# Kernel tuning notes

Hardware: AMD Instinct MI355X
Metric: run time of the kernel (lower is better)

The kernel has to match this reference:

```python
import jax, jax.numpy as jnp
import numpy as np

# Regular batched tree: BS roots, arity A, depth D (root=level 0, leaves=level D)
BS, A, D = 32, 4, 6
V, E, H = 50000, 256, 256
LEVEL_SIZES = [BS * A ** d for d in range(D + 1)]
OFFSETS = np.concatenate([[0], np.cumsum(LEVEL_SIZES)]).astype(np.int64)
TOTAL = int(OFFSETS[-1])  # 174752


def gru_cell(x, h, w_ih, w_hh, b_ih, b_hh):
    # torch nn.GRU single step, gate order (r, z, n)
    gi = x @ w_ih.T + b_ih
    gh = h @ w_hh.T + b_hh
    ir, iz, inn = jnp.split(gi, 3, axis=-1)
    hr, hz, hn = jnp.split(gh, 3, axis=-1)
    r = jax.nn.sigmoid(ir + hr)
    z = jax.nn.sigmoid(iz + hz)
    n = jnp.tanh(inn + r * hn)
    return (1.0 - z) * n + z * h


def child_attention(h_last, sent_weight, sent_bias, context_weight):
    # Reproduces hidden_per_child stacking: ch[g,c,i,:] = h_last[g,c] if c==i else 0.
    G, S, _ = h_last.shape
    eye = jnp.eye(S, dtype=h_last.dtype)
    ch = h_last[:, :, None, :] * eye[None, :, :, None]          # [G,S(c),S(i),H]
    t1 = jnp.tanh(jnp.einsum('gcih,hk->gcik', ch, sent_weight) + sent_bias[0])
    u = jnp.tanh(jnp.einsum('gcik,ko->gci', t1, context_weight))  # [G,S,S]
    w = jax.nn.softmax(u, axis=1)                                # softmax over c (the P axis)
    return jnp.einsum('gci,gcih->gih', w, ch)                    # [G,S,H]


def setup_inputs() -> dict:
    key = jax.random.key(0)
    ks = jax.random.split(key, 9)
    s = 1.0 / np.sqrt(H)
    return {
        'tokens': jax.random.randint(ks[0], (TOTAL,), 0, V, dtype=jnp.int32),
        'embedding': jax.random.normal(ks[1], (V, E), jnp.float32) * 0.1,
        'w_ih': jax.random.uniform(ks[2], (3 * H, E), jnp.float32, -s, s),
        'w_hh': jax.random.uniform(ks[3], (3 * H, H), jnp.float32, -s, s),
        'b_ih': jax.random.uniform(ks[4], (3 * H,), jnp.float32, -s, s),
        'b_hh': jax.random.uniform(ks[5], (3 * H,), jnp.float32, -s, s),
        'sent_weight': jax.random.normal(ks[6], (H, H), jnp.float32) * 0.05,
        'sent_bias': jax.random.normal(ks[7], (1, H), jnp.float32) * 0.05,
        'context_weight': jax.random.normal(ks[8], (H, 1), jnp.float32) * 0.05,
    }


def reference(tokens, embedding, w_ih, w_hh, b_ih, b_hh, sent_weight, sent_bias, context_weight):
    def tok(d):
        return tokens[int(OFFSETS[d]):int(OFFSETS[d + 1])]

    gru = lambda x, h: gru_cell(x, h, w_ih, w_hh, b_ih, b_hh)

    # leaves: no children -> zero initial hidden
    h_levels = {D: gru(embedding[tok(D)], jnp.zeros((LEVEL_SIZES[D], H), jnp.float32))}

    for d in range(D - 1, -1, -1):
        h_child = h_levels[d + 1].reshape(-1, A, H)   # [N_d, A, H]
        # duplicate index_copy in torch: only last child's hidden survives per parent
        h_last = h_child[:, A - 1, :]                 # [N_d, H]
        S = BS if d == 0 else A                       # call size: bs at root, A siblings otherwise
        groups = h_last.reshape(-1, S, H)
        chs = child_attention(groups, sent_weight, sent_bias, context_weight).reshape(-1, H)
        h_levels[d] = gru(embedding[tok(d)], chs)

    # final max over node_list: root entry has all bs rows; every other call's entry has
    # only row b = hn of the LAST sibling (duplicate valid_indices), zeros elsewhere.
    out = jnp.maximum(jnp.zeros((BS, H), jnp.float32), h_levels[0])
    for d in range(1, D + 1):
        last_sib = h_levels[d].reshape(BS, -1, A, H)[:, :, A - 1, :].max(axis=1)
        out = jnp.maximum(out, last_sib)
    return out
```

## Files before the change

kernel.cpp:

```cpp
#include <hip/hip_runtime.h>
#include <hip/hip_bf16.h>
#include <math.h>


typedef unsigned short u16;
typedef unsigned int u32;
typedef __attribute__((ext_vector_type(8))) short s8;
typedef __attribute__((ext_vector_type(4))) float f4;
#define MFMA16(a, b, c) __builtin_amdgcn_mfma_f32_16x16x32_bf16(a, b, c, 0, 0, 0)

__device__ __forceinline__ u16 f2bf(float f) {
  u32 x = __float_as_uint(f);
  return (u16)((x + 0x7fffu + ((x >> 16) & 1u)) >> 16);
}
__device__ __forceinline__ float bf2f(u16 u) { return __uint_as_float(((u32)u) << 16); }
__device__ __forceinline__ float sigmoidf_(float x) {
  return __builtin_amdgcn_rcpf(1.f + __builtin_amdgcn_exp2f(-1.4426950408889634f * x));
}
__device__ __forceinline__ float tanhf_(float x) {
  x = fminf(fmaxf(x, -15.f), 15.f);
  float t = __builtin_amdgcn_exp2f(-2.8853900817779268f * x);
  return 1.f - 2.f * t * __builtin_amdgcn_rcpf(1.f + t);
}
__device__ __forceinline__ void gload_lds16(const void* g, void* l) {
  typedef const __attribute__((address_space(1))) unsigned int* gp_t;
  typedef __attribute__((address_space(3))) unsigned int* lp_t;
  __builtin_amdgcn_global_load_lds((gp_t)g, (lp_t)l, 16, 0, 0);
}
__device__ __forceinline__ void stage_row(const float* __restrict__ emb, int tok,
                                          u16* aX, int r, int lane) {
  float4 v = ((const float4*)(emb + (size_t)tok * 256))[lane];
  uint2 val = {(u32)f2bf(v.x) | ((u32)f2bf(v.y) << 16),
               (u32)f2bf(v.z) | ((u32)f2bf(v.w) << 16)};
  *(uint2*)&aX[r * 256 + ((((lane >> 1)) ^ (r & 7)) << 3) + (lane & 1) * 4] = val;
}

__global__ void prep_pack(const float* __restrict__ wih, const float* __restrict__ whh,
                          const float* __restrict__ sw, const float* __restrict__ sb,
                          const float* __restrict__ cw,
                          u16* __restrict__ wihP, u16* __restrict__ whhPh,
                          u16* __restrict__ whhPl, u16* __restrict__ swPh,
                          float* __restrict__ u0p, int* __restrict__ outI) {
  int b = blockIdx.x, t = threadIdx.x;
  if (b == 320) {
    #pragma unroll
    for (int k = 0; k < 32; ++k) outI[k * 256 + t] = 0;
    if (t < 64) {
      float s = 0.f;
      #pragma unroll
      for (int q = 0; q < 4; ++q) { int k = t + 64 * q; s += tanhf(sb[k]) * cw[k]; }
      #pragma unroll
      for (int off = 32; off >= 1; off >>= 1) s += __shfl_xor(s, off);
      if (t == 0) u0p[0] = tanhf(s);
    }
    return;
  }
  int g = b * 256 + t;
  const float* src;
  u16* dst;
  int idx, NF, lomode, trans;
  if (g < 24576)      { idx = g;         src = wih; dst = wihP;  NF = 48; lomode = 0; trans = 1; }
  else if (g < 49152) { idx = g - 24576; src = whh; dst = whhPh; NF = 48; lomode = 0; trans = 1; }
  else if (g < 73728) { idx = g - 49152; src = whh; dst = whhPl; NF = 48; lomode = 1; trans = 1; }
  else                { idx = g - 73728; src = sw;  dst = swPh;  NF = 16; lomode = 0; trans = 0; }
  int lane = idx & 63;
  int t2 = idx >> 6;
  int nf = t2 % NF, kb = t2 / NF;
  int n = nf * 16 + (lane & 15);
  int k0 = kb * 32 + (lane >> 4) * 8;
  float v[8];
  if (trans) {
    const float4* p = (const float4*)(src + (size_t)n * 256 + k0);
    float4 a = p[0], b2 = p[1];
    v[0] = a.x; v[1] = a.y; v[2] = a.z; v[3] = a.w;
    v[4] = b2.x; v[5] = b2.y; v[6] = b2.z; v[7] = b2.w;
  } else {
    #pragma unroll
    for (int j = 0; j < 8; ++j) v[j] = src[(size_t)(k0 + j) * 256 + n];
  }
  u16 o[8];
  #pragma unroll
  for (int j = 0; j < 8; ++j) {
    u16 hi = f2bf(v[j]);
    o[j] = lomode ? f2bf(v[j] - bf2f(hi)) : hi;
  }
  u32* d = (u32*)(dst + (size_t)idx * 8);
  #pragma unroll
  for (int j = 0; j < 4; ++j) d[j] = (u32)o[2 * j] | ((u32)o[2 * j + 1] << 16);
}

__global__ __launch_bounds__(512, 2)
void levelAB_kernel(const int* __restrict__ t6, const int* __restrict__ t5,
                    const float* __restrict__ emb,
                    const u16* __restrict__ wihP, const u16* __restrict__ whhPh,
                    const u16* __restrict__ whhPl, const u16* __restrict__ swPh,
                    const float* __restrict__ bih, const float* __restrict__ bhh,
                    const float* __restrict__ sb, const float* __restrict__ cw,
                    const float* __restrict__ u0p,
                    u16* __restrict__ Hs5Hi, u16* __restrict__ Hs5Lo,
                    int* __restrict__ outI) {
  __shared__ u16 aX6[32768];
  __shared__ u16 aX5[8192];
  __shared__ u16 aH[2][8192];
  __shared__ float pm[8][32];
  __shared__ float scl[32];

  const int t = threadIdx.x;
  const int rb = blockIdx.x;
  const int lane = t & 63, w = t >> 6;
  const int asub = lane >> 4, l15 = lane & 15;
  const float LN3 = 1.0986122886681098f;
  const int batch = rb >> 3;

  {
    #pragma unroll
    for (int rr = 0; rr < 16; ++rr) {
      int r = 16 * w + rr;
      stage_row(emb, t6[4 * (128 * rb + r) + 3], aX6, r, lane);
    }
    #pragma unroll
    for (int rr = 0; rr < 4; ++rr) {
      int r = 4 * w + rr;
      stage_row(emb, t5[4 * (32 * rb + r) + 3], aX5, r, lane);
    }
  }
  __syncthreads();

  #pragma unroll 1
  for (int pass = 0; pass < 4; ++pass) {
    const int sp = pass >> 1, jc = pass & 1;
    const int cfx = 2 * w + jc;
    f4 gi[3][4];
    #pragma unroll
    for (int g = 0; g < 3; ++g)
      #pragma unroll
      for (int mf = 0; mf < 4; ++mf) gi[g][mf] = (f4){0.f, 0.f, 0.f, 0.f};
    s8 bw[2][3];
    auto LB = [&](int kb, int pb) {
      #pragma unroll
      for (int g = 0; g < 3; ++g)
        bw[pb][g] = *(const s8*)&wihP[((size_t)(kb * 48 + 16 * g + cfx) * 64 + lane) * 8];
    };
    LB(0, 0);
    #pragma unroll
    for (int kb = 0; kb < 8; ++kb) {
      const int pb = kb & 1;
      if (kb < 7) LB(kb + 1, pb ^ 1);
      s8 axh[4];
      #pragma unroll
      for (int mf = 0; mf < 4; ++mf) {
        int ab = (64 * sp + 16 * mf + l15) * 256 + (((kb * 4 + asub) ^ (l15 & 7)) << 3);
        axh[mf] = *(const s8*)&aX6[ab];
      }
      #pragma unroll
      for (int g = 0; g < 3; ++g)
        #pragma unroll
        for (int mf = 0; mf < 4; ++mf)
          gi[g][mf] = MFMA16(axh[mf], bw[pb][g], gi[g][mf]);
    }
    const int col = 16 * cfx + l15;
    const float bi0 = bih[col], bi1 = bih[256 + col], bi2 = bih[512 + col];
    const float bh0 = bhh[col], bh1 = bhh[256 + col], bh2 = bhh[512 + col];
    float cm = -1e30f;
    #pragma unroll
    for (int mf = 0; mf < 4; ++mf) {
      #pragma unroll
      for (int j = 0; j < 4; ++j) {
        float r = sigmoidf_(gi[0][mf][j] + bi0 + bh0);
        float z = sigmoidf_(gi[1][mf][j] + bi1 + bh1);
        float n = tanhf_(gi[2][mf][j] + bi2 + r * bh2);
        float h = (1.f - z) * n;
        if (j == 3) {
          int ci = 16 * sp + 4 * mf + asub;
          u16 hi = f2bf(h);
          u16 lo = f2bf(h - bf2f(hi));
          int hidx = ((col >> 3) * 32 + ci) * 8 + (col & 7);
          aH[0][hidx] = hi;
          aH[1][hidx] = lo;
        }
        cm = fmaxf(cm, h);
      }
    }
    cm = fmaxf(cm, __shfl_xor(cm, 16));
    cm = fmaxf(cm, __shfl_xor(cm, 32));
    if (asub == 0)
      atomicMax(outI + (size_t)batch * 256 + col, __float_as_int(cm));
  }
  __syncthreads();

  f4 sa[2][2];
  #pragma unroll
  for (int jc = 0; jc < 2; ++jc)
    #pragma unroll
    for (int mf = 0; mf < 2; ++mf) sa[jc][mf] = (f4){0.f, 0.f, 0.f, 0.f};
  {
    s8 bsw[2][2];
    auto LSW = [&](int kb, int pb) {
      #pragma unroll
      for (int jc = 0; jc < 2; ++jc)
        bsw[pb][jc] = *(const s8*)&swPh[((size_t)(kb * 16 + 2 * w + jc) * 64 + lane) * 8];
    };
    LSW(0, 0);
    #pragma unroll
    for (int kb = 0; kb < 8; ++kb) {
      const int pb = kb & 1;
      if (kb < 7) LSW(kb + 1, pb ^ 1);
      s8 ahh[2], ahl[2];
      #pragma unroll
      for (int mf = 0; mf < 2; ++mf) {
        int ab = ((kb * 4 + asub) * 32 + 16 * mf + l15) * 8;
        ahh[mf] = *(const s8*)&aH[0][ab];
        ahl[mf] = *(const s8*)&aH[1][ab];
      }
      #pragma unroll
      for (int jc = 0; jc < 2; ++jc) {
        sa[jc][0] = MFMA16(ahh[0], bsw[pb][jc], sa[jc][0]);
        sa[jc][1] = MFMA16(ahh[1], bsw[pb][jc], sa[jc][1]);
        sa[jc][0] = MFMA16(ahl[0], bsw[pb][jc], sa[jc][0]);
        sa[jc][1] = MFMA16(ahl[1], bsw[pb][jc], sa[jc][1]);
      }
    }
  }
  {
    float part[2][4] = {{0.f, 0.f, 0.f, 0.f}, {0.f, 0.f, 0.f, 0.f}};
    #pragma unroll
    for (int jc = 0; jc < 2; ++jc) {
      int k = 16 * (2 * w + jc) + l15;
      float sbk = sb[k], cwk = cw[k];
      #pragma unroll
      for (int mf = 0; mf < 2; ++mf)
        #pragma unroll
        for (int j = 0; j < 4; ++j) part[mf][j] += tanhf_(sa[jc][mf][j] + sbk) * cwk;
    }
    #pragma unroll
    for (int mf = 0; mf < 2; ++mf)
      #pragma unroll
      for (int j = 0; j < 4; ++j) {
        part[mf][j] += __shfl_xor(part[mf][j], 1);
        part[mf][j] += __shfl_xor(part[mf][j], 2);
        part[mf][j] += __shfl_xor(part[mf][j], 4);
        part[mf][j] += __shfl_xor(part[mf][j], 8);
      }
    if (l15 == 0) {
      #pragma unroll
      for (int mf = 0; mf < 2; ++mf)
        #pragma unroll
        for (int j = 0; j < 4; ++j) pm[w][16 * mf + 4 * asub + j] = part[mf][j];
    }
    __syncthreads();
    if (t < 32) {
      float v = 0.f;
      #pragma unroll
      for (int q = 0; q < 8; ++q) v += pm[q][t];
      scl[t] = sigmoidf_(tanhf_(v) - u0p[0] - LN3);
    }
    __syncthreads();
  }
  #pragma unroll 1
  for (int pass = 0; pass < 4; ++pass) {
    const int p = pass >> 1, mf = pass & 1;
    const int cf = w + 8 * p;
    f4 gi5[3], gh5[3];
    #pragma unroll
    for (int g = 0; g < 3; ++g) {
      gi5[g] = (f4){0.f, 0.f, 0.f, 0.f};
      gh5[g] = (f4){0.f, 0.f, 0.f, 0.f};
    }
    #pragma unroll
    for (int kb = 0; kb < 8; ++kb) {
      s8 bwi[3], bwh[3], bwl[3];
      #pragma unroll
      for (int g = 0; g < 3; ++g) {
        size_t bo = ((size_t)(kb * 48 + 16 * g + cf) * 64 + lane) * 8;
        bwi[g] = *(const s8*)&wihP[bo];
        bwh[g] = *(const s8*)&whhPh[bo];
        bwl[g] = *(const s8*)&whhPl[bo];
      }
      int axb = (16 * mf + l15) * 256 + (((kb * 4 + asub) ^ (l15 & 7)) << 3);
      s8 axh = *(const s8*)&aX5[axb];
      int ab = ((kb * 4 + asub) * 32 + 16 * mf + l15) * 8;
      s8 ahh = *(const s8*)&aH[0][ab];
      s8 ahl = *(const s8*)&aH[1][ab];
      #pragma unroll
      for (int g = 0; g < 3; ++g) {
        gi5[g] = MFMA16(axh, bwi[g], gi5[g]);
        gh5[g] = MFMA16(ahh, bwh[g], gh5[g]);
        gh5[g] = MFMA16(ahl, bwh[g], gh5[g]);
        gh5[g] = MFMA16(ahh, bwl[g], gh5[g]);
      }
    }
    const int col = 16 * cf + l15;
    const float bi0 = bih[col], bi1 = bih[256 + col], bi2 = bih[512 + col];
    const float bh0 = bhh[col], bh1 = bhh[256 + col], bh2 = bhh[512 + col];
    const int r0 = 16 * mf + 4 * asub;
    float cm = -1e30f;
    #pragma unroll
    for (int j = 0; j < 4; ++j) {
      const int row = r0 + j;
      const int i = 32 * rb + row;
      float sc = scl[row];
      float ir = gi5[0][j] + bi0;
      float iz = gi5[1][j] + bi1;
      float inn = gi5[2][j] + bi2;
      float g0 = bh0 + sc * gh5[0][j];
      float g1 = bh1 + sc * gh5[1][j];
      float g2 = bh2 + sc * gh5[2][j];
      int hidx = ((col >> 3) * 32 + row) * 8 + (col & 7);
      float hp = sc * (bf2f(aH[0][hidx]) + bf2f(aH[1][hidx]));
      float r = sigmoidf_(ir + g0);
      float z = sigmoidf_(iz + g1);
      float n = tanhf_(inn + r * g2);
      float h = (1.f - z) * n + z * hp;
      if (j == 3) {
        u16 hi = f2bf(h);
        u16 lo = f2bf(h - bf2f(hi));
        Hs5Hi[(size_t)(i >> 2) * 256 + col] = hi;
        Hs5Lo[(size_t)(i >> 2) * 256 + col] = lo;
      }
      cm = fmaxf(cm, h);
    }
    cm = fmaxf(cm, __shfl_xor(cm, 16));
    cm = fmaxf(cm, __shfl_xor(cm, 32));
    if (asub == 0)
      atomicMax(outI + (size_t)batch * 256 + col, __float_as_int(cm));
  }
}

__global__ __launch_bounds__(512, 2)
void levelB_kernel(const int* __restrict__ tokens, const float* __restrict__ emb,
                   const u16* __restrict__ wihP, const u16* __restrict__ whhPh,
                   const u16* __restrict__ whhPl, const u16* __restrict__ swPh,
                   const float* __restrict__ bih, const float* __restrict__ bhh,
                   const float* __restrict__ sb, const float* __restrict__ cw,
                   const float* __restrict__ u0p,
                   const u16* __restrict__ HpHi, const u16* __restrict__ HpLo,
                   u16* __restrict__ HoutHi, u16* __restrict__ HoutLo,
                   int* __restrict__ outI, float logSm1, int bshift) {
  __shared__ u16 aX[8192];
  __shared__ u16 aH[2][8192];
  __shared__ float pm[8][32];
  __shared__ float scl[32];

  const int t = threadIdx.x;
  const int rb = blockIdx.x >> 1, cb = blockIdx.x & 1;
  const int i0 = rb * 32;
  const int lane = t & 63, w = t >> 6;

  {
    int row = lane & 31;
    const u16* sh = HpHi + ((size_t)(i0 + row) << 8);
    const u16* sl = HpLo + ((size_t)(i0 + row) << 8);
    #pragma unroll
    for (int c = 0; c < 2; ++c) {
      int cg = w * 4 + c * 2 + (lane >> 5);
      int lb = w * 1024 + c * 512;
      gload_lds16(sh + (cg << 3), &aH[0][lb]);
      gload_lds16(sl + (cg << 3), &aH[1][lb]);
    }
  }
  {
    #pragma unroll
    for (int rr = 0; rr < 4; ++rr) {
      int r = 4 * w + rr;
      int tok = tokens[4 * (i0 + r) + 3];
      stage_row(emb, tok, aX, r, lane);
    }
  }
  __syncthreads();

  const int asub = lane >> 4, l15 = lane & 15;
  const int cfg = 8 * cb + w;

  f4 gi[3][2], gh[3][2], sa[2][2];
  #pragma unroll
  for (int g = 0; g < 3; ++g)
    #pragma unroll
    for (int mf = 0; mf < 2; ++mf) {
      gi[g][mf] = (f4){0.f, 0.f, 0.f, 0.f};
      gh[g][mf] = (f4){0.f, 0.f, 0.f, 0.f};
    }
  #pragma unroll
  for (int jc = 0; jc < 2; ++jc)
    #pragma unroll
    for (int mf = 0; mf < 2; ++mf) sa[jc][mf] = (f4){0.f, 0.f, 0.f, 0.f};

  #pragma unroll
  for (int kb = 0; kb < 8; ++kb) {
    s8 bwi[3], bwh[3], bwl[3], bsw[2];
    #pragma unroll
    for (int g = 0; g < 3; ++g) {
      size_t bo = ((size_t)(kb * 48 + 16 * g + cfg) * 64 + lane) * 8;
      bwi[g] = *(const s8*)&wihP[bo];
      bwh[g] = *(const s8*)&whhPh[bo];
      bwl[g] = *(const s8*)&whhPl[bo];
    }
    #pragma unroll
    for (int jc = 0; jc < 2; ++jc) {
      size_t so = ((size_t)(kb * 16 + 2 * w + jc) * 64 + lane) * 8;
      bsw[jc] = *(const s8*)&swPh[so];
    }
    s8 axh[2], ahh[2], ahl[2];
    #pragma unroll
    for (int mf = 0; mf < 2; ++mf) {
      int axb = (16 * mf + l15) * 256 + (((kb * 4 + asub) ^ (l15 & 7)) << 3);
      axh[mf] = *(const s8*)&aX[axb];
      int abase = ((kb * 4 + asub) * 32 + 16 * mf + l15) * 8;
      ahh[mf] = *(const s8*)&aH[0][abase];
      ahl[mf] = *(const s8*)&aH[1][abase];
    }
    #pragma unroll
    for (int g = 0; g < 3; ++g) {
      gi[g][0] = MFMA16(axh[0], bwi[g], gi[g][0]);
      gi[g][1] = MFMA16(axh[1], bwi[g], gi[g][1]);
      gh[g][0] = MFMA16(ahh[0], bwh[g], gh[g][0]);
      gh[g][1] = MFMA16(ahh[1], bwh[g], gh[g][1]);
      gh[g][0] = MFMA16(ahl[0], bwh[g], gh[g][0]);
      gh[g][1] = MFMA16(ahl[1], bwh[g], gh[g][1]);
      gh[g][0] = MFMA16(ahh[0], bwl[g], gh[g][0]);
      gh[g][1] = MFMA16(ahh[1], bwl[g], gh[g][1]);
    }
    #pragma unroll
    for (int jc = 0; jc < 2; ++jc) {
      sa[jc][0] = MFMA16(ahh[0], bsw[jc], sa[jc][0]);
      sa[jc][1] = MFMA16(ahh[1], bsw[jc], sa[jc][1]);
      sa[jc][0] = MFMA16(ahl[0], bsw[jc], sa[jc][0]);
      sa[jc][1] = MFMA16(ahl[1], bsw[jc], sa[jc][1]);
    }
  }

  {
    float part[2][4] = {{0.f, 0.f, 0.f, 0.f}, {0.f, 0.f, 0.f, 0.f}};
    #pragma unroll
    for (int jc = 0; jc < 2; ++jc) {
      int k = 16 * (2 * w + jc) + l15;
      float sbk = sb[k], cwk = cw[k];
      #pragma unroll
      for (int mf = 0; mf < 2; ++mf)
        #pragma unroll
        for (int j = 0; j < 4; ++j) part[mf][j] += tanhf_(sa[jc][mf][j] + sbk) * cwk;
    }
    #pragma unroll
    for (int mf = 0; mf < 2; ++mf)
      #pragma unroll
      for (int j = 0; j < 4; ++j) {
        part[mf][j] += __shfl_xor(part[mf][j], 1);
        part[mf][j] += __shfl_xor(part[mf][j], 2);
        part[mf][j] += __shfl_xor(part[mf][j], 4);
        part[mf][j] += __shfl_xor(part[mf][j], 8);
      }
    if (l15 == 0) {
      #pragma unroll
      for (int mf = 0; mf < 2; ++mf)
        #pragma unroll
        for (int j = 0; j < 4; ++j) pm[w][16 * mf + 4 * asub + j] = part[mf][j];
    }
    __syncthreads();
    if (t < 32) {
      float v = 0.f;
      #pragma unroll
      for (int q = 0; q < 8; ++q) v += pm[q][t];
      scl[t] = sigmoidf_(tanhf_(v) - u0p[0] - logSm1);
    }
    __syncthreads();
  }

  {
    const int col = 16 * cfg + l15;
    const float bi0 = bih[col], bi1 = bih[256 + col], bi2 = bih[512 + col];
    const float bh0 = bhh[col], bh1 = bhh[256 + col], bh2 = bhh[512 + col];
    float cmax = -1e30f;
    #pragma unroll
    for (int mf = 0; mf < 2; ++mf) {
      const int r0 = 16 * mf + 4 * asub;
      #pragma unroll
      for (int j = 0; j < 4; ++j) {
        const int row = r0 + j;
        const int i = i0 + row;
        float sc = scl[row];
        float ir = gi[0][mf][j] + bi0;
        float iz = gi[1][mf][j] + bi1;
        float inn = gi[2][mf][j] + bi2;
        float g0 = bh0 + sc * gh[0][mf][j];
        float g1 = bh1 + sc * gh[1][mf][j];
        float g2 = bh2 + sc * gh[2][mf][j];
        int hidx = ((col >> 3) * 32 + row) * 8 + (col & 7);
        float hp = sc * (bf2f(aH[0][hidx]) + bf2f(aH[1][hidx]));
        float r = sigmoidf_(ir + g0);
        float z = sigmoidf_(iz + g1);
        float n = tanhf_(inn + r * g2);
        float h = (1.f - z) * n + z * hp;
        if ((i & 3) == 3) {
          u16 hi = f2bf(h);
          u16 lo = f2bf(h - bf2f(hi));
          HoutHi[(size_t)(i >> 2) * 256 + col] = hi;
          HoutLo[(size_t)(i >> 2) * 256 + col] = lo;
        }
        cmax = fmaxf(cmax, h);
      }
    }
    cmax = fmaxf(cmax, __shfl_xor(cmax, 16));
    cmax = fmaxf(cmax, __shfl_xor(cmax, 32));
    if (asub == 0)
      atomicMax(outI + (size_t)(i0 >> bshift) * 256 + col, __float_as_int(cmax));
  }
}

__device__ __forceinline__ void level16(
    const u16* __restrict__ aXp, const u16* __restrict__ aHh,
    const u16* __restrict__ aHl,
    const u16* __restrict__ wihP, const u16* __restrict__ whhPh,
    const u16* __restrict__ whhPl, const u16* __restrict__ swPh,
    const float* __restrict__ bih, const float* __restrict__ bhh,
    const float* __restrict__ sb, const float* __restrict__ cw, float u0v,
    float logSm1, int nvalid, u16* outHh, u16* outHl, int outMode,
    int* __restrict__ outI, int mode, int batchBase,
    float (*pm)[32], float* scl, int t) {
  const int lane = t & 63, w = t >> 6;
  const int asub = lane >> 4, l15 = lane & 15;
  f4 sa0 = (f4){0.f, 0.f, 0.f, 0.f}, sa1 = (f4){0.f, 0.f, 0.f, 0.f};
  #pragma unroll
  for (int kb = 0; kb < 8; ++kb) {
    s8 b0 = *(const s8*)&swPh[((size_t)(kb * 16 + 2 * w) * 64 + lane) * 8];
    s8 b1 = *(const s8*)&swPh[((size_t)(kb * 16 + 2 * w + 1) * 64 + lane) * 8];
    int ab = ((kb * 4 + asub) * 16 + l15) * 8;
    s8 ahh = *(const s8*)&aHh[ab];
    s8 ahl = *(const s8*)&aHl[ab];
    sa0 = MFMA16(ahh, b0, sa0); sa0 = MFMA16(ahl, b0, sa0);
    sa1 = MFMA16(ahh, b1, sa1); sa1 = MFMA16(ahl, b1, sa1);
  }
  {
    float part[4] = {0.f, 0.f, 0.f, 0.f};
    #pragma unroll
    for (int jc = 0; jc < 2; ++jc) {
      int k = 16 * (2 * w + jc) + l15;
      float sbk = sb[k], cwk = cw[k];
      #pragma unroll
      for (int j = 0; j < 4; ++j)
        part[j] += tanhf_((jc ? sa1[j] : sa0[j]) + sbk) * cwk;
    }
    #pragma unroll
    for (int j = 0; j < 4; ++j) {
      part[j] += __shfl_xor(part[j], 1);
      part[j] += __shfl_xor(part[j], 2);
      part[j] += __shfl_xor(part[j], 4);
      part[j] += __shfl_xor(part[j], 8);
    }
    if (l15 == 0) {
      #pragma unroll
      for (int j = 0; j < 4; ++j) pm[w][4 * asub + j] = part[j];
    }
    __syncthreads();
    if (t < 16) {
      float v = 0.f;
      #pragma unroll
      for (int q = 0; q < 8; ++q) v += pm[q][t];
      scl[t] = sigmoidf_(tanhf_(v) - u0v - logSm1);
    }
    __syncthreads();
  }
  #pragma unroll 1
  for (int p = 0; p < 2; ++p) {
    const int cf = w + 8 * p;
    f4 gi5[3], gh5[3];
    #pragma unroll
    for (int g = 0; g < 3; ++g) {
      gi5[g] = (f4){0.f, 0.f, 0.f, 0.f};
      gh5[g] = (f4){0.f, 0.f, 0.f, 0.f};
    }
    #pragma unroll
    for (int kb = 0; kb < 8; ++kb) {
      s8 bwi[3], bwh[3], bwl[3];
      #pragma unroll
      for (int g = 0; g < 3; ++g) {
        size_t bo = ((size_t)(kb * 48 + 16 * g + cf) * 64 + lane) * 8;
        bwi[g] = *(const s8*)&wihP[bo];
        bwh[g] = *(const s8*)&whhPh[bo];
        bwl[g] = *(const s8*)&whhPl[bo];
      }
      int axb = l15 * 256 + (((kb * 4 + asub) ^ (l15 & 7)) << 3);
      s8 axh = *(const s8*)&aXp[axb];
      int ab = ((kb * 4 + asub) * 16 + l15) * 8;
      s8 ahh = *(const s8*)&aHh[ab];
      s8 ahl = *(const s8*)&aHl[ab];
      #pragma unroll
      for (int g = 0; g < 3; ++g) {
        gi5[g] = MFMA16(axh, bwi[g], gi5[g]);
        gh5[g] = MFMA16(ahh, bwh[g], gh5[g]);
        gh5[g] = MFMA16(ahl, bwh[g], gh5[g]);
        gh5[g] = MFMA16(ahh, bwl[g], gh5[g]);
      }
    }
    const int col = 16 * cf + l15;
    const float bi0 = bih[col], bi1 = bih[256 + col], bi2 = bih[512 + col];
    const float bh0 = bhh[col], bh1 = bhh[256 + col], bh2 = bhh[512 + col];
    float cm = -1e30f;
    #pragma unroll
    for (int j = 0; j < 4; ++j) {
      const int row = 4 * asub + j;
      const int valid = row < nvalid;
      float sc = scl[row];
      float ir = gi5[0][j] + bi0;
      float iz = gi5[1][j] + bi1;
      float inn = gi5[2][j] + bi2;
      float g0 = bh0 + sc * gh5[0][j];
      float g1 = bh1 + sc * gh5[1][j];
      float g2 = bh2 + sc * gh5[2][j];
      int hix = ((col >> 3) * 16 + row) * 8 + (col & 7);
      float hp = sc * (bf2f(aHh[hix]) + bf2f(aHl[hix]));
      float r = sigmoidf_(ir + g0);
      float z = sigmoidf_(iz + g1);
      float n = tanhf_(inn + r * g2);
      float h = (1.f - z) * n + z * hp;
      u16 hi = f2bf(h);
      u16 lo = f2bf(h - bf2f(hi));
      if (outMode == 1 && j == 3 && valid) {
        int ho = ((col >> 3) * 16 + asub) * 8 + (col & 7);
        outHh[ho] = hi; outHl[ho] = lo;
      } else if (outMode == 2 && valid) {
        outHh[hix] = hi; outHl[hix] = lo;
      }
      if (mode == 2) {
        if (valid)
          atomicMax(outI + (size_t)(batchBase + row) * 256 + col, __float_as_int(h));
      } else if (valid) {
        cm = fmaxf(cm, h);
      }
    }
    if (mode == 0) {
      cm = fmaxf(cm, __shfl_xor(cm, 16));
      cm = fmaxf(cm, __shfl_xor(cm, 32));
      if (asub == 0)
        atomicMax(outI + (size_t)batchBase * 256 + col, __float_as_int(cm));
    }
  }
}

__global__ __launch_bounds__(512, 2)
void tailF2_kernel(const int* __restrict__ t3, const int* __restrict__ t2,
                   const int* __restrict__ t1, const int* __restrict__ t0,
                   const float* __restrict__ emb,
                   const u16* __restrict__ wihP, const u16* __restrict__ whhPh,
                   const u16* __restrict__ whhPl, const u16* __restrict__ swPh,
                   const float* __restrict__ bih, const float* __restrict__ bhh,
                   const float* __restrict__ sb, const float* __restrict__ cw,
                   const float* __restrict__ u0p,
                   const u16* __restrict__ Hs4Hi, const u16* __restrict__ Hs4Lo,
                   int* __restrict__ outI) {
  __shared__ u16 aX3[4096], aH3h[4096], aH3l[4096];
  __shared__ u16 aX2[4096], aH2h[4096], aH2l[4096];
  __shared__ u16 aX1[4096], aH1h[4096], aH1l[4096];
  __shared__ u16 aX0[4096], aH0h[4096], aH0l[4096];
  __shared__ float pm[8][32];
  __shared__ float scl[32];

  const int t = threadIdx.x, b = blockIdx.x;
  const int lane = t & 63, w = t >> 6;
  const float LN3 = 1.0986122886681098f;
  const float LN31 = 3.4339872044851463f;
  const float u0v = u0p[0];

  {
    int row = t & 15, kg = t >> 4;
    uint4 vh = *(const uint4*)&Hs4Hi[(size_t)(16 * b + row) * 256 + kg * 8];
    uint4 vl = *(const uint4*)&Hs4Lo[(size_t)(16 * b + row) * 256 + kg * 8];
    *(uint4*)&aH3h[(kg * 16 + row) * 8] = vh;
    *(uint4*)&aH3l[(kg * 16 + row) * 8] = vl;
    stage_row(emb, t3[4 * (16 * b + w) + 3], aX3, w, lane);
    stage_row(emb, t3[4 * (16 * b + w + 8) + 3], aX3, w + 8, lane);
    if (w < 4) stage_row(emb, t2[4 * (4 * b + w) + 3], aX2, w, lane);
    if (w == 4) stage_row(emb, t1[4 * b + 3], aX1, 0, lane);
    if (w == 5) stage_row(emb, t0[b], aX0, 0, lane);
  }
  __syncthreads();

  level16(aX3, aH3h, aH3l, wihP, whhPh, whhPl, swPh, bih, bhh, sb, cw, u0v,
          LN3, 16, aH2h, aH2l, 1, outI, 0, b, pm, scl, t);
  __syncthreads();
  level16(aX2, aH2h, aH2l, wihP, whhPh, whhPl, swPh, bih, bhh, sb, cw, u0v,
          LN3, 4, aH1h, aH1l, 1, outI, 0, b, pm, scl, t);
  __syncthreads();
  level16(aX1, aH1h, aH1l, wihP, whhPh, whhPl, swPh, bih, bhh, sb, cw, u0v,
          LN3, 1, aH0h, aH0l, 2, outI, 2, b, pm, scl, t);
  __syncthreads();
  level16(aX0, aH0h, aH0l, wihP, whhPh, whhPl, swPh, bih, bhh, sb, cw, u0v,
          LN31, 1, nullptr, nullptr, 0, outI, 2, b, pm, scl, t);
}

extern "C" void kernel_launch(void* const* d_in, const int* in_sizes, int n_in,
                              void* d_out, int out_size, void* d_ws, size_t ws_size,
                              hipStream_t stream) {
  const int*   tokens = (const int*)d_in[0];
  const float* emb    = (const float*)d_in[1];
  const float* wih    = (const float*)d_in[2];
  const float* whh    = (const float*)d_in[3];
  const float* bih    = (const float*)d_in[4];
  const float* bhh    = (const float*)d_in[5];
  const float* sw     = (const float*)d_in[6];
  const float* sb     = (const float*)d_in[7];
  const float* cw     = (const float*)d_in[8];

  char* ws = (char*)d_ws;
  u16* wihP  = (u16*)(ws + 0);
  u16* whhPh = (u16*)(ws + 393216);
  u16* whhPl = (u16*)(ws + 786432);
  u16* swPh  = (u16*)(ws + 1179648);
  float* u0p = (float*)(ws + 1310720);
  u16* Hs5Hi = (u16*)(ws + 9961472);
  u16* Hs5Lo = (u16*)(ws + 11010048);
  u16* Hs4Hi = (u16*)(ws + 12058624);
  u16* Hs4Lo = (u16*)(ws + 12320768);

  int* outI = (int*)d_out;
  prep_pack<<<321, 256, 0, stream>>>(wih, whh, sw, sb, cw,
                                     wihP, whhPh, whhPl, swPh, u0p, outI);

  const float LN3 = 1.0986122886681098f;

  levelAB_kernel<<<256, 512, 0, stream>>>(
      tokens + 43680, tokens + 10912, emb, wihP, whhPh, whhPl, swPh,
      bih, bhh, sb, cw, u0p, Hs5Hi, Hs5Lo, outI);
  levelB_kernel<<<128, 512, 0, stream>>>(
      tokens + 2720, emb, wihP, whhPh, whhPl, swPh, bih, bhh, sb, cw, u0p,
      Hs5Hi, Hs5Lo, Hs4Hi, Hs4Lo, outI, LN3, 6);
  tailF2_kernel<<<32, 512, 0, stream>>>(
      tokens + 672, tokens + 160, tokens + 32, tokens, emb,
      wihP, whhPh, whhPl, swPh, bih, bhh, sb, cw, u0p, Hs4Hi, Hs4Lo, outI);
}
```

Measured before the change: 122.7 us.

## Halve levelAB block work and double grid, reuse level16 helper for level five

```diff
diff --git a/kernel.cpp b/kernel.cpp
--- a/kernel.cpp
+++ b/kernel.cpp
@@ -89,7 +89,141 @@
   for (int j = 0; j < 4; ++j) d[j] = (u32)o[2 * j] | ((u32)o[2 * j + 1] << 16);
 }
 
-__global__ __launch_bounds__(512, 2)
+__device__ __forceinline__ void level16(
+    const u16* __restrict__ aXp, const u16* __restrict__ aHh,
+    const u16* __restrict__ aHl,
+    const u16* __restrict__ wihP, const u16* __restrict__ whhPh,
+    const u16* __restrict__ whhPl, const u16* __restrict__ swPh,
+    const float* __restrict__ bih, const float* __restrict__ bhh,
+    const float* __restrict__ sb, const float* __restrict__ cw, float u0v,
+    float logSm1, int nvalid, u16* outHh, u16* outHl, int outMode,
+    u16* __restrict__ gHi, u16* __restrict__ gLo, int gBase,
+    int* __restrict__ outI, int mode, int batchBase,
+    float (*pm)[32], float* scl, int t) {
+  const int lane = t & 63, w = t >> 6;
+  const int asub = lane >> 4, l15 = lane & 15;
+  f4 sa0 = (f4){0.f, 0.f, 0.f, 0.f}, sa1 = (f4){0.f, 0.f, 0.f, 0.f};
+  #pragma unroll
+  for (int kb = 0; kb < 8; ++kb) {
+    s8 b0 = *(const s8*)&swPh[((size_t)(kb * 16 + 2 * w) * 64 + lane) * 8];
+    s8 b1 = *(const s8*)&swPh[((size_t)(kb * 16 + 2 * w + 1) * 64 + lane) * 8];
+    int ab = ((kb * 4 + asub) * 16 + l15) * 8;
+    s8 ahh = *(const s8*)&aHh[ab];
+    s8 ahl = *(const s8*)&aHl[ab];
+    sa0 = MFMA16(ahh, b0, sa0); sa0 = MFMA16(ahl, b0, sa0);
+    sa1 = MFMA16(ahh, b1, sa1); sa1 = MFMA16(ahl, b1, sa1);
+  }
+  {
+    float part[4] = {0.f, 0.f, 0.f, 0.f};
+    #pragma unroll
+    for (int jc = 0; jc < 2; ++jc) {
+      int k = 16 * (2 * w + jc) + l15;
+      float sbk = sb[k], cwk = cw[k];
+      #pragma unroll
+      for (int j = 0; j < 4; ++j)
+        part[j] += tanhf_((jc ? sa1[j] : sa0[j]) + sbk) * cwk;
+    }
+    #pragma unroll
+    for (int j = 0; j < 4; ++j) {
+      part[j] += __shfl_xor(part[j], 1);
+      part[j] += __shfl_xor(part[j], 2);
+      part[j] += __shfl_xor(part[j], 4);
+      part[j] += __shfl_xor(part[j], 8);
+    }
+    if (l15 == 0) {
+      #pragma unroll
+      for (int j = 0; j < 4; ++j) pm[w][4 * asub + j] = part[j];
+    }
+    __syncthreads();
+    if (t < 16) {
+      float v = 0.f;
+      #pragma unroll
+      for (int q = 0; q < 8; ++q) v += pm[q][t];
+      scl[t] = sigmoidf_(tanhf_(v) - u0v - logSm1);
+    }
+    __syncthreads();
+  }
+  #pragma unroll 1
+  for (int p = 0; p < 2; ++p) {
+    const int cf = w + 8 * p;
+    f4 gi5[3], gh5[3];
+    #pragma unroll
+    for (int g = 0; g < 3; ++g) {
+      gi5[g] = (f4){0.f, 0.f, 0.f, 0.f};
+      gh5[g] = (f4){0.f, 0.f, 0.f, 0.f};
+    }
+    #pragma unroll
+    for (int kb = 0; kb < 8; ++kb) {
+      s8 bwi[3], bwh[3], bwl[3];
+      #pragma unroll
+      for (int g = 0; g < 3; ++g) {
+        size_t bo = ((size_t)(kb * 48 + 16 * g + cf) * 64 + lane) * 8;
+        bwi[g] = *(const s8*)&wihP[bo];
+        bwh[g] = *(const s8*)&whhPh[bo];
+        bwl[g] = *(const s8*)&whhPl[bo];
+      }
+      int axb = l15 * 256 + (((kb * 4 + asub) ^ (l15 & 7)) << 3);
+      s8 axh = *(const s8*)&aXp[axb];
+      int ab = ((kb * 4 + asub) * 16 + l15) * 8;
+      s8 ahh = *(const s8*)&aHh[ab];
+      s8 ahl = *(const s8*)&aHl[ab];
+      #pragma unroll
+      for (int g = 0; g < 3; ++g) {
+        gi5[g] = MFMA16(axh, bwi[g], gi5[g]);
+        gh5[g] = MFMA16(ahh, bwh[g], gh5[g]);
+        gh5[g] = MFMA16(ahl, bwh[g], gh5[g]);
+        gh5[g] = MFMA16(ahh, bwl[g], gh5[g]);
+      }
+    }
+    const int col = 16 * cf + l15;
+    const float bi0 = bih[col], bi1 = bih[256 + col], bi2 = bih[512 + col];
+    const float bh0 = bhh[col], bh1 = bhh[256 + col], bh2 = bhh[512 + col];
+    float cm = -1e30f;
+    #pragma unroll
+    for (int j = 0; j < 4; ++j) {
+      const int row = 4 * asub + j;
+      const int valid = row < nvalid;
+      float sc = scl[row];
+      float ir = gi5[0][j] + bi0;
+      float iz = gi5[1][j] + bi1;
+      float inn = gi5[2][j] + bi2;
+      float g0 = bh0 + sc * gh5[0][j];
+      float g1 = bh1 + sc * gh5[1][j];
+      float g2 = bh2 + sc * gh5[2][j];
+      int hix = ((col >> 3) * 16 + row) * 8 + (col & 7);
+      float hp = sc * (bf2f(aHh[hix]) + bf2f(aHl[hix]));
+      float r = sigmoidf_(ir + g0);
+      float z = sigmoidf_(iz + g1);
+      float n = tanhf_(inn + r * g2);
+      float h = (1.f - z) * n + z * hp;
+      u16 hi = f2bf(h);
+      u16 lo = f2bf(h - bf2f(hi));
+      if (outMode == 1 && j == 3 && valid) {
+        int ho = ((col >> 3) * 16 + asub) * 8 + (col & 7);
+        outHh[ho] = hi; outHl[ho] = lo;
+      } else if (outMode == 2 && valid) {
+        outHh[hix] = hi; outHl[hix] = lo;
+      } else if (outMode == 3 && j == 3 && valid) {
+        gHi[(size_t)(gBase + asub) * 256 + col] = hi;
+        gLo[(size_t)(gBase + asub) * 256 + col] = lo;
+      }
+      if (mode == 2) {
+        if (valid)
+          atomicMax(outI + (size_t)(batchBase + row) * 256 + col, __float_as_int(h));
+      } else if (valid) {
+        cm = fmaxf(cm, h);
+      }
+    }
+    if (mode == 0) {
+      cm = fmaxf(cm, __shfl_xor(cm, 16));
+      cm = fmaxf(cm, __shfl_xor(cm, 32));
+      if (asub == 0)
+        atomicMax(outI + (size_t)batchBase * 256 + col, __float_as_int(cm));
+    }
+  }
+}
+
+__global__ __launch_bounds__(512, 4)
 void levelAB_kernel(const int* __restrict__ t6, const int* __restrict__ t5,
                     const float* __restrict__ emb,
                     const u16* __restrict__ wihP, const u16* __restrict__ whhPh,
@@ -99,9 +233,9 @@
                     const float* __restrict__ u0p,
                     u16* __restrict__ Hs5Hi, u16* __restrict__ Hs5Lo,
                     int* __restrict__ outI) {
-  __shared__ u16 aX6[32768];
-  __shared__ u16 aX5[8192];
-  __shared__ u16 aH[2][8192];
+  __shared__ u16 aX6[16384];
+  __shared__ u16 aX5[4096];
+  __shared__ u16 aHh[4096], aHl[4096];
   __shared__ float pm[8][32];
   __shared__ float scl[32];
 
@@ -110,25 +244,24 @@
   const int lane = t & 63, w = t >> 6;
   const int asub = lane >> 4, l15 = lane & 15;
   const float LN3 = 1.0986122886681098f;
-  const int batch = rb >> 3;
-
-  {
-    #pragma unroll
-    for (int rr = 0; rr < 16; ++rr) {
-      int r = 16 * w + rr;
-      stage_row(emb, t6[4 * (128 * rb + r) + 3], aX6, r, lane);
-    }
-    #pragma unroll
-    for (int rr = 0; rr < 4; ++rr) {
-      int r = 4 * w + rr;
-      stage_row(emb, t5[4 * (32 * rb + r) + 3], aX5, r, lane);
+  const int batch = rb >> 4;
+
+  {
+    #pragma unroll
+    for (int rr = 0; rr < 8; ++rr) {
+      int r = 8 * w + rr;
+      stage_row(emb, t6[4 * (64 * rb + r) + 3], aX6, r, lane);
+    }
+    #pragma unroll
+    for (int rr = 0; rr < 2; ++rr) {
+      int r = 2 * w + rr;
+      stage_row(emb, t5[4 * (16 * rb + r) + 3], aX5, r, lane);
     }
   }
   __syncthreads();
 
   #pragma unroll 1
-  for (int pass = 0; pass < 4; ++pass) {
-    const int sp = pass >> 1, jc = pass & 1;
+  for (int jc = 0; jc < 2; ++jc) {
     const int cfx = 2 * w + jc;
     f4 gi[3][4];
     #pragma unroll
@@ -149,7 +282,7 @@
       s8 axh[4];
       #pragma unroll
       for (int mf = 0; mf < 4; ++mf) {
-        int ab = (64 * sp + 16 * mf + l15) * 256 + (((kb * 4 + asub) ^ (l15 & 7)) << 3);
+        int ab = (16 * mf + l15) * 256 + (((kb * 4 + asub) ^ (l15 & 7)) << 3);
         axh[mf] = *(const s8*)&aX6[ab];
       }
       #pragma unroll
@@ -171,12 +304,12 @@
         float n = tanhf_(gi[2][mf][j] + bi2 + r * bh2);
         float h = (1.f - z) * n;
         if (j == 3) {
-          int ci = 16 * sp + 4 * mf + asub;
+          int ci = 4 * mf + asub;
           u16 hi = f2bf(h);
           u16 lo = f2bf(h - bf2f(hi));
-          int hidx = ((col >> 3) * 32 + ci) * 8 + (col & 7);
-          aH[0][hidx] = hi;
-          aH[1][hidx] = lo;
+          int hidx = ((col >> 3) * 16 + ci) * 8 + (col & 7);
+          aHh[hidx] = hi;
+          aHl[hidx] = lo;
         }
         cm = fmaxf(cm, h);
       }
@@ -188,142 +321,9 @@
   }
   __syncthreads();
 
-  f4 sa[2][2];
-  #pragma unroll
-  for (int jc = 0; jc < 2; ++jc)
-    #pragma unroll
-    for (int mf = 0; mf < 2; ++mf) sa[jc][mf] = (f4){0.f, 0.f, 0.f, 0.f};
-  {
-    s8 bsw[2][2];
-    auto LSW = [&](int kb, int pb) {
-      #pragma unroll
-      for (int jc = 0; jc < 2; ++jc)
-        bsw[pb][jc] = *(const s8*)&swPh[((size_t)(kb * 16 + 2 * w + jc) * 64 + lane) * 8];
-    };
-    LSW(0, 0);
-    #pragma unroll
-    for (int kb = 0; kb < 8; ++kb) {
-      const int pb = kb & 1;
-      if (kb < 7) LSW(kb + 1, pb ^ 1);
-      s8 ahh[2], ahl[2];
-      #pragma unroll
-      for (int mf = 0; mf < 2; ++mf) {
-        int ab = ((kb * 4 + asub) * 32 + 16 * mf + l15) * 8;
-        ahh[mf] = *(const s8*)&aH[0][ab];
-        ahl[mf] = *(const s8*)&aH[1][ab];
-      }
-      #pragma unroll
-      for (int jc = 0; jc < 2; ++jc) {
-        sa[jc][0] = MFMA16(ahh[0], bsw[pb][jc], sa[jc][0]);
-        sa[jc][1] = MFMA16(ahh[1], bsw[pb][jc], sa[jc][1]);
-        sa[jc][0] = MFMA16(ahl[0], bsw[pb][jc], sa[jc][0]);
-        sa[jc][1] = MFMA16(ahl[1], bsw[pb][jc], sa[jc][1]);
-      }
-    }
-  }
-  {
-    float part[2][4] = {{0.f, 0.f, 0.f, 0.f}, {0.f, 0.f, 0.f, 0.f}};
-    #pragma unroll
-    for (int jc = 0; jc < 2; ++jc) {
-      int k = 16 * (2 * w + jc) + l15;
-      float sbk = sb[k], cwk = cw[k];
-      #pragma unroll
-      for (int mf = 0; mf < 2; ++mf)
-        #pragma unroll
-        for (int j = 0; j < 4; ++j) part[mf][j] += tanhf_(sa[jc][mf][j] + sbk) * cwk;
-    }
-    #pragma unroll
-    for (int mf = 0; mf < 2; ++mf)
-      #pragma unroll
-      for (int j = 0; j < 4; ++j) {
-        part[mf][j] += __shfl_xor(part[mf][j], 1);
-        part[mf][j] += __shfl_xor(part[mf][j], 2);
-        part[mf][j] += __shfl_xor(part[mf][j], 4);
-        part[mf][j] += __shfl_xor(part[mf][j], 8);
-      }
-    if (l15 == 0) {
-      #pragma unroll
-      for (int mf = 0; mf < 2; ++mf)
-        #pragma unroll
-        for (int j = 0; j < 4; ++j) pm[w][16 * mf + 4 * asub + j] = part[mf][j];
-    }
-    __syncthreads();
-    if (t < 32) {
-      float v = 0.f;
-      #pragma unroll
-      for (int q = 0; q < 8; ++q) v += pm[q][t];
-      scl[t] = sigmoidf_(tanhf_(v) - u0p[0] - LN3);
-    }
-    __syncthreads();
-  }
-  #pragma unroll 1
-  for (int pass = 0; pass < 4; ++pass) {
-    const int p = pass >> 1, mf = pass & 1;
-    const int cf = w + 8 * p;
-    f4 gi5[3], gh5[3];
-    #pragma unroll
-    for (int g = 0; g < 3; ++g) {
-      gi5[g] = (f4){0.f, 0.f, 0.f, 0.f};
-      gh5[g] = (f4){0.f, 0.f, 0.f, 0.f};
-    }
-    #pragma unroll
-    for (int kb = 0; kb < 8; ++kb) {
-      s8 bwi[3], bwh[3], bwl[3];
-      #pragma unroll
-      for (int g = 0; g < 3; ++g) {
-        size_t bo = ((size_t)(kb * 48 + 16 * g + cf) * 64 + lane) * 8;
-        bwi[g] = *(const s8*)&wihP[bo];
-        bwh[g] = *(const s8*)&whhPh[bo];
-        bwl[g] = *(const s8*)&whhPl[bo];
-      }
-      int axb = (16 * mf + l15) * 256 + (((kb * 4 + asub) ^ (l15 & 7)) << 3);
-      s8 axh = *(const s8*)&aX5[axb];
-      int ab = ((kb * 4 + asub) * 32 + 16 * mf + l15) * 8;
-      s8 ahh = *(const s8*)&aH[0][ab];
-      s8 ahl = *(const s8*)&aH[1][ab];
-      #pragma unroll
-      for (int g = 0; g < 3; ++g) {
-        gi5[g] = MFMA16(axh, bwi[g], gi5[g]);
-        gh5[g] = MFMA16(ahh, bwh[g], gh5[g]);
-        gh5[g] = MFMA16(ahl, bwh[g], gh5[g]);
-        gh5[g] = MFMA16(ahh, bwl[g], gh5[g]);
-      }
-    }
-    const int col = 16 * cf + l15;
-    const float bi0 = bih[col], bi1 = bih[256 + col], bi2 = bih[512 + col];
-    const float bh0 = bhh[col], bh1 = bhh[256 + col], bh2 = bhh[512 + col];
-    const int r0 = 16 * mf + 4 * asub;
-    float cm = -1e30f;
-    #pragma unroll
-    for (int j = 0; j < 4; ++j) {
-      const int row = r0 + j;
-      const int i = 32 * rb + row;
-      float sc = scl[row];
-      float ir = gi5[0][j] + bi0;
-      float iz = gi5[1][j] + bi1;
-      float inn = gi5[2][j] + bi2;
-      float g0 = bh0 + sc * gh5[0][j];
-      float g1 = bh1 + sc * gh5[1][j];
-      float g2 = bh2 + sc * gh5[2][j];
-      int hidx = ((col >> 3) * 32 + row) * 8 + (col & 7);
-      float hp = sc * (bf2f(aH[0][hidx]) + bf2f(aH[1][hidx]));
-      float r = sigmoidf_(ir + g0);
-      float z = sigmoidf_(iz + g1);
-      float n = tanhf_(inn + r * g2);
-      float h = (1.f - z) * n + z * hp;
-      if (j == 3) {
-        u16 hi = f2bf(h);
-        u16 lo = f2bf(h - bf2f(hi));
-        Hs5Hi[(size_t)(i >> 2) * 256 + col] = hi;
-        Hs5Lo[(size_t)(i >> 2) * 256 + col] = lo;
-      }
-      cm = fmaxf(cm, h);
-    }
-    cm = fmaxf(cm, __shfl_xor(cm, 16));
-    cm = fmaxf(cm, __shfl_xor(cm, 32));
-    if (asub == 0)
-      atomicMax(outI + (size_t)batch * 256 + col, __float_as_int(cm));
-  }
+  level16(aX5, aHh, aHl, wihP, whhPh, whhPl, swPh, bih, bhh, sb, cw, u0p[0],
+          LN3, 16, nullptr, nullptr, 3, Hs5Hi, Hs5Lo, 4 * rb,
+          outI, 0, batch, pm, scl, t);
 }
 
 __global__ __launch_bounds__(512, 2)
@@ -505,136 +505,6 @@
   }
 }
 
-__device__ __forceinline__ void level16(
-    const u16* __restrict__ aXp, const u16* __restrict__ aHh,
-    const u16* __restrict__ aHl,
-    const u16* __restrict__ wihP, const u16* __restrict__ whhPh,
-    const u16* __restrict__ whhPl, const u16* __restrict__ swPh,
-    const float* __restrict__ bih, const float* __restrict__ bhh,
-    const float* __restrict__ sb, const float* __restrict__ cw, float u0v,
-    float logSm1, int nvalid, u16* outHh, u16* outHl, int outMode,
-    int* __restrict__ outI, int mode, int batchBase,
-    float (*pm)[32], float* scl, int t) {
-  const int lane = t & 63, w = t >> 6;
-  const int asub = lane >> 4, l15 = lane & 15;
-  f4 sa0 = (f4){0.f, 0.f, 0.f, 0.f}, sa1 = (f4){0.f, 0.f, 0.f, 0.f};
-  #pragma unroll
-  for (int kb = 0; kb < 8; ++kb) {
-    s8 b0 = *(const s8*)&swPh[((size_t)(kb * 16 + 2 * w) * 64 + lane) * 8];
-    s8 b1 = *(const s8*)&swPh[((size_t)(kb * 16 + 2 * w + 1) * 64 + lane) * 8];
-    int ab = ((kb * 4 + asub) * 16 + l15) * 8;
-    s8 ahh = *(const s8*)&aHh[ab];
-    s8 ahl = *(const s8*)&aHl[ab];
-    sa0 = MFMA16(ahh, b0, sa0); sa0 = MFMA16(ahl, b0, sa0);
-    sa1 = MFMA16(ahh, b1, sa1); sa1 = MFMA16(ahl, b1, sa1);
-  }
-  {
-    float part[4] = {0.f, 0.f, 0.f, 0.f};
-    #pragma unroll
-    for (int jc = 0; jc < 2; ++jc) {
-      int k = 16 * (2 * w + jc) + l15;
-      float sbk = sb[k], cwk = cw[k];
-      #pragma unroll
-      for (int j = 0; j < 4; ++j)
-        part[j] += tanhf_((jc ? sa1[j] : sa0[j]) + sbk) * cwk;
-    }
-    #pragma unroll
-    for (int j = 0; j < 4; ++j) {
-      part[j] += __shfl_xor(part[j], 1);
-      part[j] += __shfl_xor(part[j], 2);
-      part[j] += __shfl_xor(part[j], 4);
-      part[j] += __shfl_xor(part[j], 8);
-    }
-    if (l15 == 0) {
-      #pragma unroll
-      for (int j = 0; j < 4; ++j) pm[w][4 * asub + j] = part[j];
-    }
-    __syncthreads();
-    if (t < 16) {
-      float v = 0.f;
-      #pragma unroll
-      for (int q = 0; q < 8; ++q) v += pm[q][t];
-      scl[t] = sigmoidf_(tanhf_(v) - u0v - logSm1);
-    }
-    __syncthreads();
-  }
-  #pragma unroll 1
-  for (int p = 0; p < 2; ++p) {
-    const int cf = w + 8 * p;
-    f4 gi5[3], gh5[3];
-    #pragma unroll
-    for (int g = 0; g < 3; ++g) {
-      gi5[g] = (f4){0.f, 0.f, 0.f, 0.f};
-      gh5[g] = (f4){0.f, 0.f, 0.f, 0.f};
-    }
-    #pragma unroll
-    for (int kb = 0; kb < 8; ++kb) {
-      s8 bwi[3], bwh[3], bwl[3];
-      #pragma unroll
-      for (int g = 0; g < 3; ++g) {
-        size_t bo = ((size_t)(kb * 48 + 16 * g + cf) * 64 + lane) * 8;
-        bwi[g] = *(const s8*)&wihP[bo];
-        bwh[g] = *(const s8*)&whhPh[bo];
-        bwl[g] = *(const s8*)&whhPl[bo];
-      }
-      int axb = l15 * 256 + (((kb * 4 + asub) ^ (l15 & 7)) << 3);
-      s8 axh = *(const s8*)&aXp[axb];
-      int ab = ((kb * 4 + asub) * 16 + l15) * 8;
-      s8 ahh = *(const s8*)&aHh[ab];
-      s8 ahl = *(const s8*)&aHl[ab];
-      #pragma unroll
-      for (int g = 0; g < 3; ++g) {
-        gi5[g] = MFMA16(axh, bwi[g], gi5[g]);
-        gh5[g] = MFMA16(ahh, bwh[g], gh5[g]);
-        gh5[g] = MFMA16(ahl, bwh[g], gh5[g]);
-        gh5[g] = MFMA16(ahh, bwl[g], gh5[g]);
-      }
-    }
-    const int col = 16 * cf + l15;
-    const float bi0 = bih[col], bi1 = bih[256 + col], bi2 = bih[512 + col];
-    const float bh0 = bhh[col], bh1 = bhh[256 + col], bh2 = bhh[512 + col];
-    float cm = -1e30f;
-    #pragma unroll
-    for (int j = 0; j < 4; ++j) {
-      const int row = 4 * asub + j;
-      const int valid = row < nvalid;
-      float sc = scl[row];
-      float ir = gi5[0][j] + bi0;
-      float iz = gi5[1][j] + bi1;
-      float inn = gi5[2][j] + bi2;
-      float g0 = bh0 + sc * gh5[0][j];
-      float g1 = bh1 + sc * gh5[1][j];
-      float g2 = bh2 + sc * gh5[2][j];
-      int hix = ((col >> 3) * 16 + row) * 8 + (col & 7);
-      float hp = sc * (bf2f(aHh[hix]) + bf2f(aHl[hix]));
-      float r = sigmoidf_(ir + g0);
-      float z = sigmoidf_(iz + g1);
-      float n = tanhf_(inn + r * g2);
-      float h = (1.f - z) * n + z * hp;
-      u16 hi = f2bf(h);
-      u16 lo = f2bf(h - bf2f(hi));
-      if (outMode == 1 && j == 3 && valid) {
-        int ho = ((col >> 3) * 16 + asub) * 8 + (col & 7);
-        outHh[ho] = hi; outHl[ho] = lo;
-      } else if (outMode == 2 && valid) {
-        outHh[hix] = hi; outHl[hix] = lo;
-      }
-      if (mode == 2) {
-        if (valid)
-          atomicMax(outI + (size_t)(batchBase + row) * 256 + col, __float_as_int(h));
-      } else if (valid) {
-        cm = fmaxf(cm, h);
-      }
-    }
-    if (mode == 0) {
-      cm = fmaxf(cm, __shfl_xor(cm, 16));
-      cm = fmaxf(cm, __shfl_xor(cm, 32));
-      if (asub == 0)
-        atomicMax(outI + (size_t)batchBase * 256 + col, __float_as_int(cm));
-    }
-  }
-}
-
 __global__ __launch_bounds__(512, 2)
 void tailF2_kernel(const int* __restrict__ t3, const int* __restrict__ t2,
                    const int* __restrict__ t1, const int* __restrict__ t0,
@@ -674,16 +544,16 @@
   __syncthreads();
 
   level16(aX3, aH3h, aH3l, wihP, whhPh, whhPl, swPh, bih, bhh, sb, cw, u0v,
-          LN3, 16, aH2h, aH2l, 1, outI, 0, b, pm, scl, t);
+          LN3, 16, aH2h, aH2l, 1, nullptr, nullptr, 0, outI, 0, b, pm, scl, t);
   __syncthreads();
   level16(aX2, aH2h, aH2l, wihP, whhPh, whhPl, swPh, bih, bhh, sb, cw, u0v,
-          LN3, 4, aH1h, aH1l, 1, outI, 0, b, pm, scl, t);
+          LN3, 4, aH1h, aH1l, 1, nullptr, nullptr, 0, outI, 0, b, pm, scl, t);
   __syncthreads();
   level16(aX1, aH1h, aH1l, wihP, whhPh, whhPl, swPh, bih, bhh, sb, cw, u0v,
-          LN3, 1, aH0h, aH0l, 2, outI, 2, b, pm, scl, t);
+          LN3, 1, aH0h, aH0l, 2, nullptr, nullptr, 0, outI, 2, b, pm, scl, t);
   __syncthreads();
   level16(aX0, aH0h, aH0l, wihP, whhPh, whhPl, swPh, bih, bhh, sb, cw, u0v,
-          LN31, 1, nullptr, nullptr, 0, outI, 2, b, pm, scl, t);
+          LN31, 1, nullptr, nullptr, 0, nullptr, nullptr, 0, outI, 2, b, pm, scl, t);
 }
 
 extern "C" void kernel_launch(void* const* d_in, const int* in_sizes, int n_in,
@@ -716,7 +586,7 @@
 
   const float LN3 = 1.0986122886681098f;
 
-  levelAB_kernel<<<256, 512, 0, stream>>>(
+  levelAB_kernel<<<512, 512, 0, stream>>>(
       tokens + 43680, tokens + 10912, emb, wihP, whhPh, whhPl, swPh,
       bih, bhh, sb, cw, u0p, Hs5Hi, Hs5Lo, outI);
   levelB_kernel<<<128, 512, 0, stream>>>(
```

Measured after the change: 189.7 us. 1.55x slower.
